# Performance work log

Hardware: AMD Instinct MI355X
Metric: run time of the kernel (lower is better)

The kernel has to match this reference:

```python
import jax, jax.numpy as jnp
import numpy as np
from jax import lax

B, L, D = 2, 512, 1024
N, K, R = 16, 4, 64
DEPTH, V, MLP = 4, 50000, 4096
HALF = D // 2


def _ln(x, s, b, eps=1e-5):
    m = x.mean(-1, keepdims=True)
    v = ((x - m) ** 2).mean(-1, keepdims=True)
    return (x - m) / jnp.sqrt(v + eps) * s + b


def _selective_scan(x, wx, wz, wp, cw, dtw, dtb, a_log, dpar, wout):
    bsz, seqlen, d = x.shape
    x_res = x @ wx.T
    z = x @ wz.T
    p = x @ wp.T  # [B,L,R+2N]
    dt_u, b_proj, c_proj = p[..., :R], p[..., R:R + N], p[..., R + N:]
    dt = jax.nn.softplus(dt_u @ dtw.T + dtb)  # [B,L,D]
    # causal depthwise conv (torch pads K-1 both sides then slices :L == left-pad K-1)
    conv = lax.conv_general_dilated(x_res.transpose(0, 2, 1), cw[:, None, :],
                                    (1,), [(K - 1, 0)], feature_group_count=d)
    u = jax.nn.silu(conv.transpose(0, 2, 1))  # [B,L,D]
    a = -jnp.exp(a_log)  # [D,N]
    a_t = jnp.exp(dt[..., None] * a)  # [B,L,D,N] (ZOH discretize)
    b_t = jnp.where(jnp.abs(a) < 1e-8, dt[..., None], (a_t - 1.0) / (a + 1e-10))
    inp = b_t * b_proj[:, :, None, :] * u[..., None]  # [B,L,D,N]

    def step(h, xs):
        at, it, ct = xs
        h = at * h + it
        return h, jnp.einsum('bn,bdn->bd', ct, h)

    h0 = jnp.zeros((bsz, d, N), a_t.dtype)
    _, ys = lax.scan(step, h0, (a_t.transpose(1, 0, 2, 3),
                                inp.transpose(1, 0, 2, 3),
                                c_proj.transpose(1, 0, 2)))
    y = ys.transpose(1, 0, 2)  # [B,L,D]
    y = (y + u * dpar) * jax.nn.silu(z)
    return y @ wout.T


def _forward(input_ids, timesteps, emb_table, tw1, tb1, tw2, tb2,
             ln1_s, ln1_b, wx, wz, wp, conv_w, dt_w, dt_b, A_log, Dp, wout,
             ln2_s, ln2_b, mlp_w1, mlp_b1, mlp_w2, mlp_b2,
             lnout_s, lnout_b, head_w, head_b):
    # sinusoidal time embedding [B,D]
    freq = jnp.exp(jnp.arange(HALF, dtype=jnp.float32) * (-np.log(10000.0) / (HALF - 1)))
    e = timesteps.astype(jnp.float32)[:, None] * freq
    temb = jnp.concatenate([jnp.sin(e), jnp.cos(e)], axis=-1)
    temb = jax.nn.silu(temb @ tw1.T + tb1) @ tw2.T + tb2
    x = emb_table[input_ids] + temb[:, None, :]
    for i in range(DEPTH):
        h = _selective_scan(_ln(x, ln1_s[i], ln1_b[i]), wx[i], wz[i], wp[i],
                            conv_w[i], dt_w[i], dt_b[i], A_log[i], Dp[i], wout[i])
        x = x + h
        m = _ln(x, ln2_s[i], ln2_b[i])
        m = jax.nn.gelu(m @ mlp_w1[i].T + mlp_b1[i], approximate=False) @ mlp_w2[i].T + mlp_b2[i]
        x = x + m
    x = _ln(x, lnout_s, lnout_b)
    return x @ head_w.T + head_b  # [B,L,V]


def setup_inputs() -> dict:
    key = jax.random.key(0)
    ks = jax.random.split(key, 20)

    def nrm(k, shape, scale=0.02):
        return jax.random.normal(k, shape, jnp.float32) * scale

    dt_std = R ** (-0.5)
    inp = {
        'input_ids': jax.random.randint(ks[0], (B, L), 0, V + 1),
        'timesteps': jax.random.randint(ks[1], (B,), 0, 100),
        'emb_table': nrm(ks[2], (V + 1, D)),
        'tw1': nrm(ks[3], (4 * D, D)), 'tb1': jnp.zeros((4 * D,), jnp.float32),
        'tw2': nrm(ks[4], (D, 4 * D)), 'tb2': jnp.zeros((D,), jnp.float32),
        'ln1_s': jnp.ones((DEPTH, D), jnp.float32), 'ln1_b': jnp.zeros((DEPTH, D), jnp.float32),
        'wx': nrm(ks[5], (DEPTH, D, D)),
        'wz': nrm(ks[6], (DEPTH, D, D)),
        'wp': nrm(ks[7], (DEPTH, R + 2 * N, D)),
        'conv_w': nrm(ks[8], (DEPTH, D, K), 0.1),
        'dt_w': jax.random.uniform(ks[9], (DEPTH, D, R), jnp.float32, -dt_std, dt_std),
        'dt_b': jnp.full((DEPTH, D), float(np.log(np.expm1(0.01))), jnp.float32),
        'A_log': jnp.tile(jnp.log(jnp.arange(1, N + 1, dtype=jnp.float32))[None, None, :], (DEPTH, D, 1)),
        'Dp': jnp.ones((DEPTH, D), jnp.float32),
        'wout': nrm(ks[10], (DEPTH, D, D)),
        'ln2_s': jnp.ones((DEPTH, D), jnp.float32), 'ln2_b': jnp.zeros((DEPTH, D), jnp.float32),
        'mlp_w1': nrm(ks[11], (DEPTH, MLP, D)), 'mlp_b1': jnp.zeros((DEPTH, MLP), jnp.float32),
        'mlp_w2': nrm(ks[12], (DEPTH, D, MLP)), 'mlp_b2': jnp.zeros((DEPTH, D), jnp.float32),
        'lnout_s': jnp.ones((D,), jnp.float32), 'lnout_b': jnp.zeros((D,), jnp.float32),
        'head_w': nrm(ks[13], (V, D)), 'head_b': jnp.zeros((V,), jnp.float32),
    }
    return inp


def reference(input_ids, timesteps, emb_table, tw1, tb1, tw2, tb2,
              ln1_s, ln1_b, wx, wz, wp, conv_w, dt_w, dt_b, A_log, Dp, wout,
              ln2_s, ln2_b, mlp_w1, mlp_b1, mlp_w2, mlp_b2,
              lnout_s, lnout_b, head_w, head_b):
    return _forward(input_ids, timesteps, emb_table, tw1, tb1, tw2, tb2,
                    ln1_s, ln1_b, wx, wz, wp, conv_w, dt_w, dt_b, A_log, Dp, wout,
                    ln2_s, ln2_b, mlp_w1, mlp_b1, mlp_w2, mlp_b2,
                    lnout_s, lnout_b, head_w, head_b)
```

## Files before the change

kernel.cpp:

```cpp
#include <hip/hip_runtime.h>

typedef unsigned short u16;
typedef __attribute__((ext_vector_type(8))) __bf16 bf16x8;
typedef __attribute__((ext_vector_type(4))) float floatx4;

#define B_ 2
#define L_ 512
#define D_ 1024
#define N_ 16
#define R_ 64
#define DEPTH_ 4
#define V_ 50000
#define MLP_ 4096
#define MROWS (B_ * L_)
#define SCAN_C 32
#define SCAN_S (L_ / SCAN_C)

#define SWZ(b) ((b) ^ ((((b) >> 7) & 7) << 4))

__device__ __forceinline__ u16 f2b(float f) {
    return __builtin_bit_cast(u16, (__bf16)f);
}
__device__ __forceinline__ uint2 f4_to_b4(float4 v) {
    u16 a = f2b(v.x), b = f2b(v.y), c = f2b(v.z), d = f2b(v.w);
    uint2 r;
    r.x = (unsigned int)a | ((unsigned int)b << 16);
    r.y = (unsigned int)c | ((unsigned int)d << 16);
    return r;
}
__device__ __forceinline__ void async16(const void* g, void* l) {
    __builtin_amdgcn_global_load_lds(
        (const __attribute__((address_space(1))) void*)g,
        (__attribute__((address_space(3))) void*)l, 16, 0, 0);
}
template <int Ncnt>
__device__ __forceinline__ void waitcnt_vm() {
    if constexpr (Ncnt == 0) asm volatile("s_waitcnt vmcnt(0)" ::: "memory");
    else if constexpr (Ncnt == 2) asm volatile("s_waitcnt vmcnt(2)" ::: "memory");
    else if constexpr (Ncnt == 3) asm volatile("s_waitcnt vmcnt(3)" ::: "memory");
    else if constexpr (Ncnt == 4) asm volatile("s_waitcnt vmcnt(4)" ::: "memory");
    else if constexpr (Ncnt == 5) asm volatile("s_waitcnt vmcnt(5)" ::: "memory");
    else if constexpr (Ncnt == 6) asm volatile("s_waitcnt vmcnt(6)" ::: "memory");
    else if constexpr (Ncnt == 8) asm volatile("s_waitcnt vmcnt(8)" ::: "memory");
    else asm volatile("s_waitcnt vmcnt(0)" ::: "memory");
}
__device__ __forceinline__ float silu_f(float v) { return v / (1.f + expf(-v)); }
__device__ __forceinline__ float gelu_f(float v) {
    return 0.5f * v * (1.f + erff(v * 0.7071067811865476f));
}
__device__ __forceinline__ float softplus_f(float v) {
    return fmaxf(v, 0.f) + log1pf(expf(-fabsf(v)));
}

__global__ __launch_bounds__(256) void cvt_kernel(const float* __restrict__ in,
                                                  u16* __restrict__ out, const int n8) {
    const int i = blockIdx.x * 256 + threadIdx.x;
    if (i >= n8) return;
    const float4 a = *reinterpret_cast<const float4*>(&in[(size_t)i * 8]);
    const float4 b = *reinterpret_cast<const float4*>(&in[(size_t)i * 8 + 4]);
    uint4 o;
    uint2 lo = f4_to_b4(a), hi = f4_to_b4(b);
    o.x = lo.x; o.y = lo.y; o.z = hi.x; o.w = hi.y;
    *reinterpret_cast<uint4*>(&out[(size_t)i * 8]) = o;
}

template <int BM, int BN, int ACT, int RES, typename AT, typename WT, typename OUT>
__global__ __launch_bounds__(256) void gemm_bt(
    const AT* __restrict__ A, const int lda,
    const WT* __restrict__ W, const WT* __restrict__ W2,
    const float* __restrict__ bias,
    OUT* __restrict__ out, OUT* __restrict__ out2,
    const int N, const int K, const int nt) {
    constexpr int BK = 64;
    constexpr int MI = BM / 32;
    constexpr int NI = BN / 32;
    constexpr int WM = BM / 2;
    constexpr bool PIPE = (sizeof(AT) == 2) && (sizeof(WT) == 2);
    __shared__ alignas(16) u16 lA[(PIPE ? 2 : 1) * BM * BK];
    __shared__ alignas(16) u16 lW[(PIPE ? 2 : 1) * BN * BK];
    const int tid = threadIdx.x;
    const int lane = tid & 63, wv = tid >> 6;
    const int bid = blockIdx.x;
    const int m0 = (bid / nt) * BM;
    int n0 = (bid % nt) * BN;
    const WT* Wp = W;
    OUT* op = out;
    if (W2 != nullptr && n0 >= N) {
        Wp = W2;
        op = out2;
        n0 -= N;
    }
    const int wr = wv >> 1, wc = wv & 1;
    const int lr = lane & 15, kg = lane >> 4;

    floatx4 acc[MI][NI];
#pragma unroll
    for (int i = 0; i < MI; ++i)
#pragma unroll
        for (int j = 0; j < NI; ++j) {
            floatx4 z4 = {0.f, 0.f, 0.f, 0.f};
            acc[i][j] = z4;
        }

    const int T = K / BK;

    if constexpr (PIPE) {
        constexpr int NEWER = BM / 32 + BN / 32;
        auto issue = [&](int t) {
            const int buf = t & 1;
            const int kt = t * BK;
#pragma unroll
            for (int c = wv; c < BM / 8; c += 4) {
                const int dst = c * 1024 + lane * 16;
                const int lg = SWZ(dst);
                const int row = lg >> 7, colb = lg & 127;
                async16((const char*)A + ((size_t)(m0 + row) * lda + kt) * 2 + colb,
                        (char*)lA + buf * BM * 128 + c * 1024);
            }
#pragma unroll
            for (int c = wv; c < BN / 8; c += 4) {
                const int dst = c * 1024 + lane * 16;
                const int lg = SWZ(dst);
                const int row = lg >> 7, colb = lg & 127;
                int rn = n0 + row;
                rn = (rn < N) ? rn : (N - 1);
                async16((const char*)Wp + ((size_t)rn * K + kt) * 2 + colb,
                        (char*)lW + buf * BN * 128 + c * 1024);
            }
        };
        issue(0);
        for (int t = 0; t < T; ++t) {
            if (t + 1 < T) {
                issue(t + 1);
                waitcnt_vm<NEWER>();
            } else {
                waitcnt_vm<0>();
            }
            __builtin_amdgcn_s_barrier();
            __builtin_amdgcn_sched_barrier(0);
            const char* bA = (const char*)lA + (t & 1) * BM * 128;
            const char* bW = (const char*)lW + (t & 1) * BN * 128;
#pragma unroll
            for (int kk = 0; kk < 2; ++kk) {
                bf16x8 aF[MI], bF[NI];
#pragma unroll
                for (int mi = 0; mi < MI; ++mi)
                    aF[mi] = *reinterpret_cast<const bf16x8*>(
                        bA + SWZ((wr * WM + mi * 16 + lr) * 128 + kk * 64 + kg * 16));
#pragma unroll
                for (int ni = 0; ni < NI; ++ni)
                    bF[ni] = *reinterpret_cast<const bf16x8*>(
                        bW + SWZ((wc * (BN / 2) + ni * 16 + lr) * 128 + kk * 64 + kg * 16));
#pragma unroll
                for (int mi = 0; mi < MI; ++mi)
#pragma unroll
                    for (int ni = 0; ni < NI; ++ni)
                        acc[mi][ni] = __builtin_amdgcn_mfma_f32_16x16x32_bf16(
                            aF[mi], bF[ni], acc[mi][ni], 0, 0, 0);
            }
            __builtin_amdgcn_sched_barrier(0);
            if (t + 1 < T) __builtin_amdgcn_s_barrier();
        }
    } else {
        for (int t = 0; t < T; ++t) {
            const int kt = t * BK;
            if (t) __syncthreads();
            if constexpr (sizeof(AT) == 2) {
#pragma unroll
                for (int c = wv; c < BM / 8; c += 4) {
                    const int dst = c * 1024 + lane * 16;
                    const int lg = SWZ(dst);
                    const int row = lg >> 7, colb = lg & 127;
                    async16((const char*)A + ((size_t)(m0 + row) * lda + kt) * 2 + colb,
                            (char*)lA + c * 1024);
                }
            } else {
                constexpr int ACHF = (BM * BK) / 1024;
                float4 raF[ACHF];
#pragma unroll
                for (int i = 0; i < ACHF; ++i) {
                    const int idx = tid + i * 256;
                    const int row = idx >> 4, c4 = (idx & 15) * 4;
                    raF[i] = *reinterpret_cast<const float4*>(&A[(size_t)(m0 + row) * lda + kt + c4]);
                }
#pragma unroll
                for (int i = 0; i < ACHF; ++i) {
                    const int idx = tid + i * 256;
                    const int row = idx >> 4, c4 = (idx & 15) * 4;
                    *reinterpret_cast<uint2*>((char*)lA + SWZ(row * 128 + c4 * 2)) = f4_to_b4(raF[i]);
                }
            }
            if constexpr (sizeof(WT) == 2) {
#pragma unroll
                for (int c = wv; c < BN / 8; c += 4) {
                    const int dst = c * 1024 + lane * 16;
                    const int lg = SWZ(dst);
                    const int row = lg >> 7, colb = lg & 127;
                    int rn = n0 + row;
                    rn = (rn < N) ? rn : (N - 1);
                    async16((const char*)Wp + ((size_t)rn * K + kt) * 2 + colb,
                            (char*)lW + c * 1024);
                }
            } else {
                constexpr int WCHF = (BN * BK) / 1024;
                float4 rwF[WCHF];
#pragma unroll
                for (int i = 0; i < WCHF; ++i) {
                    const int idx = tid + i * 256;
                    const int row = idx >> 4, c4 = (idx & 15) * 4;
                    int rn = n0 + row;
                    rn = (rn < N) ? rn : (N - 1);
                    rwF[i] = *reinterpret_cast<const float4*>(&Wp[(size_t)rn * K + kt + c4]);
                }
#pragma unroll
                for (int i = 0; i < WCHF; ++i) {
                    const int idx = tid + i * 256;
                    const int row = idx >> 4, c4 = (idx & 15) * 4;
                    *reinterpret_cast<uint2*>((char*)lW + SWZ(row * 128 + c4 * 2)) = f4_to_b4(rwF[i]);
                }
            }
            __syncthreads();
#pragma unroll
            for (int kk = 0; kk < 2; ++kk) {
                bf16x8 aF[MI], bF[NI];
#pragma unroll
                for (int mi = 0; mi < MI; ++mi)
                    aF[mi] = *reinterpret_cast<const bf16x8*>(
                        (const char*)lA + SWZ((wr * WM + mi * 16 + lr) * 128 + kk * 64 + kg * 16));
#pragma unroll
                for (int ni = 0; ni < NI; ++ni)
                    bF[ni] = *reinterpret_cast<const bf16x8*>(
                        (const char*)lW + SWZ((wc * (BN / 2) + ni * 16 + lr) * 128 + kk * 64 + kg * 16));
#pragma unroll
                for (int mi = 0; mi < MI; ++mi)
#pragma unroll
                    for (int ni = 0; ni < NI; ++ni)
                        acc[mi][ni] = __builtin_amdgcn_mfma_f32_16x16x32_bf16(
                            aF[mi], bF[ni], acc[mi][ni], 0, 0, 0);
            }
        }
    }

#pragma unroll
    for (int mi = 0; mi < MI; ++mi) {
        const int rb = m0 + wr * WM + mi * 16 + kg * 4;
#pragma unroll
        for (int r = 0; r < 4; ++r) {
            const size_t rowoff = (size_t)(rb + r) * (size_t)N;
#pragma unroll
            for (int ni = 0; ni < NI; ++ni) {
                const int col = n0 + wc * (BN / 2) + ni * 16 + lr;
                if (col >= N) continue;
                float v = acc[mi][ni][r] + (bias ? bias[col] : 0.f);
                if constexpr (ACT == 1) v = gelu_f(v);
                if constexpr (ACT == 2) v = softplus_f(v);
                const size_t o = rowoff + (size_t)col;
                if constexpr (RES) {
                    op[o] += v;
                } else if constexpr (sizeof(OUT) == 2) {
                    op[o] = f2b(v);
                } else {
                    op[o] = v;
                }
            }
        }
    }
}

__global__ __launch_bounds__(256) void temb0_kernel(const int* __restrict__ ts,
                                                    float* __restrict__ temb0) {
    int i = blockIdx.x * 256 + threadIdx.x;
    if (i >= B_ * D_) return;
    int b = i >> 10, k = i & 1023;
    float t = (float)ts[b];
    int h = (k < 512) ? k : (k - 512);
    float f = expf((float)h * (-9.210340371976184f / 511.f));
    float e = t * f;
    temb0[i] = (k < 512) ? sinf(e) : cosf(e);
}

template <int ACTV>
__global__ __launch_bounds__(256) void rowdot_kernel(const float* __restrict__ in,
                                                     const float* __restrict__ W,
                                                     const float* __restrict__ bias,
                                                     float* __restrict__ out,
                                                     const int Ncols, const int K) {
    const int g = (blockIdx.x * 256 + threadIdx.x) >> 6;
    const int lane = threadIdx.x & 63;
    if (g >= B_ * Ncols) return;
    const int b = g / Ncols, j = g % Ncols;
    const float* xr = in + (size_t)b * K;
    const float* wr = W + (size_t)j * K;
    float s = 0.f;
    for (int k = lane; k < K; k += 64) s += xr[k] * wr[k];
#pragma unroll
    for (int o = 32; o; o >>= 1) s += __shfl_xor(s, o);
    if (lane == 0) {
        float v = s + bias[j];
        if (ACTV == 1) v = silu_f(v);
        out[(size_t)b * Ncols + j] = v;
    }
}

__global__ __launch_bounds__(256) void embed_kernel(const int* __restrict__ ids,
                                                    const float* __restrict__ emb,
                                                    const float* __restrict__ temb2,
                                                    float* __restrict__ x) {
    const int gid = blockIdx.x * 256 + threadIdx.x;
    const int d8 = gid & 127;
    const int row = gid >> 7;
    const int b = row >> 9;
    const int d0 = d8 * 8;
    const int id = ids[row];
    const float4 e0 = *reinterpret_cast<const float4*>(&emb[(size_t)id * D_ + d0]);
    const float4 e1 = *reinterpret_cast<const float4*>(&emb[(size_t)id * D_ + d0 + 4]);
    const float4 t0 = *reinterpret_cast<const float4*>(&temb2[b * D_ + d0]);
    const float4 t1 = *reinterpret_cast<const float4*>(&temb2[b * D_ + d0 + 4]);
    float4 o0, o1;
    o0.x = e0.x + t0.x; o0.y = e0.y + t0.y; o0.z = e0.z + t0.z; o0.w = e0.w + t0.w;
    o1.x = e1.x + t1.x; o1.y = e1.y + t1.y; o1.z = e1.z + t1.z; o1.w = e1.w + t1.w;
    *reinterpret_cast<float4*>(&x[(size_t)row * D_ + d0]) = o0;
    *reinterpret_cast<float4*>(&x[(size_t)row * D_ + d0 + 4]) = o1;
}

__global__ __launch_bounds__(256) void ln_kernel(const float* __restrict__ x,
                                                 const float* __restrict__ s,
                                                 const float* __restrict__ bb,
                                                 u16* __restrict__ out) {
    __shared__ float red[4];
    const int row = blockIdx.x, tid = threadIdx.x;
    const float4 v = *reinterpret_cast<const float4*>(x + (size_t)row * D_ + tid * 4);
    float sm = v.x + v.y + v.z + v.w;
#pragma unroll
    for (int o = 1; o < 64; o <<= 1) sm += __shfl_xor(sm, o);
    if ((tid & 63) == 0) red[tid >> 6] = sm;
    __syncthreads();
    const float mean = (red[0] + red[1] + red[2] + red[3]) * (1.f / 1024.f);
    __syncthreads();
    const float dx = v.x - mean, dy = v.y - mean, dz = v.z - mean, dw = v.w - mean;
    float sq = dx * dx + dy * dy + dz * dz + dw * dw;
#pragma unroll
    for (int o = 1; o < 64; o <<= 1) sq += __shfl_xor(sq, o);
    if ((tid & 63) == 0) red[tid >> 6] = sq;
    __syncthreads();
    const float var = (red[0] + red[1] + red[2] + red[3]) * (1.f / 1024.f);
    const float rs = rsqrtf(var + 1e-5f);
    const int c = tid * 4;
    const float4 sv = *reinterpret_cast<const float4*>(&s[c]);
    const float4 bv = *reinterpret_cast<const float4*>(&bb[c]);
    float4 o;
    o.x = dx * rs * sv.x + bv.x;
    o.y = dy * rs * sv.y + bv.y;
    o.z = dz * rs * sv.z + bv.z;
    o.w = dw * rs * sv.w + bv.w;
    *reinterpret_cast<uint2*>(&out[(size_t)row * D_ + c]) = f4_to_b4(o);
}

__global__ __launch_bounds__(256) void conv_silu_kernel(const float* __restrict__ xres,
                                                        const float* __restrict__ cw,
                                                        float* __restrict__ u) {
    const int gid = blockIdx.x * 256 + threadIdx.x;
    const int d4 = gid & 255;
    const int row = gid >> 8;
    const int t = row & 511;
    const int b = row >> 9;
    const int d0 = d4 * 4;
    float wj[4][4];
#pragma unroll
    for (int j = 0; j < 4; ++j) {
        const float4 w4 = *reinterpret_cast<const float4*>(&cw[(d0 + j) * 4]);
        wj[j][0] = w4.x; wj[j][1] = w4.y; wj[j][2] = w4.z; wj[j][3] = w4.w;
    }
    float acc[4] = {};
#pragma unroll
    for (int k = 0; k < 4; ++k) {
        const int tt = t - 3 + k;
        if (tt < 0) continue;
        const float4 xv = *reinterpret_cast<const float4*>(&xres[(size_t)(b * L_ + tt) * D_ + d0]);
        acc[0] += xv.x * wj[0][k];
        acc[1] += xv.y * wj[1][k];
        acc[2] += xv.z * wj[2][k];
        acc[3] += xv.w * wj[3][k];
    }
    float4 o;
    o.x = silu_f(acc[0]); o.y = silu_f(acc[1]); o.z = silu_f(acc[2]); o.w = silu_f(acc[3]);
    *reinterpret_cast<float4*>(&u[(size_t)row * D_ + d0]) = o;
}

__global__ __launch_bounds__(256) void scan_p1(const float* __restrict__ dt,
                                               const float* __restrict__ p,
                                               const float* __restrict__ u,
                                               const float* __restrict__ alog,
                                               float* __restrict__ Aprod,
                                               float* __restrict__ Hloc) {
    const int tid = threadIdx.x;
    const int ng = tid & 3;
    const int dl = tid >> 2;
    int blk = blockIdx.x;
    const int chunk = blk % SCAN_C; blk /= SCAN_C;
    const int dg = blk % (D_ / 64);
    const int b = blk / (D_ / 64);
    const int d = dg * 64 + dl;

    float a_v[4], inv_a[4];
#pragma unroll
    for (int j = 0; j < 4; ++j) {
        float av = -expf(alog[d * N_ + ng * 4 + j]);
        a_v[j] = av;
        inv_a[j] = 1.f / (av + 1e-10f);
    }

    __shared__ float pbuf[SCAN_S * 32];
    const int t0 = chunk * SCAN_S;
    if (tid < SCAN_S * 8) {
        const int s = tid >> 3, off = (tid & 7) * 4;
        *reinterpret_cast<float4*>(&pbuf[s * 32 + off]) =
            *reinterpret_cast<const float4*>(&p[((size_t)(b * L_ + t0 + s)) * 96 + 64 + off]);
    }
    __syncthreads();

    float A[4] = {1.f, 1.f, 1.f, 1.f};
    float h[4] = {0.f, 0.f, 0.f, 0.f};
#pragma unroll
    for (int s = 0; s < SCAN_S; ++s) {
        const size_t idx = ((size_t)(b * L_ + t0 + s)) * D_ + d;
        const float dtv = dt[idx];
        const float uv = u[idx];
#pragma unroll
        for (int j = 0; j < 4; ++j) {
            const float ex = fminf(dtv * a_v[j], 0.f);
            const float at = expf(ex);
            const float bt = (fabsf(a_v[j]) < 1e-8f) ? dtv : (at - 1.f) * inv_a[j];
            const float bp = pbuf[s * 32 + ng * 4 + j];
            A[j] *= at;
            h[j] = at * h[j] + bt * bp * uv;
        }
    }
    const size_t o = ((size_t)(b * SCAN_C + chunk) * D_ + d) * N_ + ng * 4;
    float4 a4 = {A[0], A[1], A[2], A[3]};
    float4 h4 = {h[0], h[1], h[2], h[3]};
    *reinterpret_cast<float4*>(&Aprod[o]) = a4;
    *reinterpret_cast<float4*>(&Hloc[o]) = h4;
}

__global__ __launch_bounds__(256) void scan_p2(const float* __restrict__ Aprod,
                                               const float* __restrict__ Hloc,
                                               float* __restrict__ Hstart) {
    const int gid = blockIdx.x * 256 + threadIdx.x;
    if (gid >= B_ * D_ * N_) return;
    const int b = gid / (D_ * N_);
    const int rem = gid % (D_ * N_);
    float H = 0.f;
#pragma unroll 8
    for (int k = 0; k < SCAN_C; ++k) {
        const size_t o = (size_t)(b * SCAN_C + k) * (D_ * N_) + rem;
        Hstart[o] = H;
        H = Aprod[o] * H + Hloc[o];
    }
}

__global__ __launch_bounds__(256) void scan_p3(const float* __restrict__ dt,
                                               const float* __restrict__ p,
                                               const float* __restrict__ u,
                                               const float* __restrict__ z,
                                               const float* __restrict__ alog,
                                               const float* __restrict__ Dp,
                                               const float* __restrict__ Hstart,
                                               u16* __restrict__ yg) {
    const int tid = threadIdx.x;
    const int ng = tid & 3;
    const int dl = tid >> 2;
    int blk = blockIdx.x;
    const int chunk = blk % SCAN_C; blk /= SCAN_C;
    const int dg = blk % (D_ / 64);
    const int b = blk / (D_ / 64);
    const int d = dg * 64 + dl;

    float a_v[4], inv_a[4];
#pragma unroll
    for (int j = 0; j < 4; ++j) {
        float av = -expf(alog[d * N_ + ng * 4 + j]);
        a_v[j] = av;
        inv_a[j] = 1.f / (av + 1e-10f);
    }
    const float Dpd = Dp[d];

    __shared__ float pbuf[SCAN_S * 32];
    const int t0 = chunk * SCAN_S;
    if (tid < SCAN_S * 8) {
        const int s = tid >> 3, off = (tid & 7) * 4;
        *reinterpret_cast<float4*>(&pbuf[s * 32 + off]) =
            *reinterpret_cast<const float4*>(&p[((size_t)(b * L_ + t0 + s)) * 96 + 64 + off]);
    }
    __syncthreads();

    float h[4];
    {
        const size_t o = ((size_t)(b * SCAN_C + chunk) * D_ + d) * N_ + ng * 4;
        const float4 h4 = *reinterpret_cast<const float4*>(&Hstart[o]);
        h[0] = h4.x; h[1] = h4.y; h[2] = h4.z; h[3] = h4.w;
    }

#pragma unroll
    for (int s = 0; s < SCAN_S; ++s) {
        const size_t idx = ((size_t)(b * L_ + t0 + s)) * D_ + d;
        const float dtv = dt[idx];
        const float uv = u[idx];
        float yp = 0.f;
#pragma unroll
        for (int j = 0; j < 4; ++j) {
            const float ex = fminf(dtv * a_v[j], 0.f);
            const float at = expf(ex);
            const float bt = (fabsf(a_v[j]) < 1e-8f) ? dtv : (at - 1.f) * inv_a[j];
            const float bp = pbuf[s * 32 + ng * 4 + j];
            const float cp = pbuf[s * 32 + 16 + ng * 4 + j];
            h[j] = at * h[j] + bt * bp * uv;
            yp += cp * h[j];
        }
        yp += __shfl_xor(yp, 1);
        yp += __shfl_xor(yp, 2);
        if (ng == 0) {
            const float zv = z[idx];
            yg[idx] = f2b((yp + uv * Dpd) * silu_f(zv));
        }
    }
}

extern "C" void kernel_launch(void* const* d_in, const int* in_sizes, int n_in,
                              void* d_out, int out_size, void* d_ws, size_t ws_size,
                              hipStream_t stream) {
    (void)in_sizes; (void)n_in; (void)out_size;
    const int* ids = (const int*)d_in[0];
    const int* tsteps = (const int*)d_in[1];
    const float* emb = (const float*)d_in[2];
    const float* tw1 = (const float*)d_in[3];
    const float* tb1 = (const float*)d_in[4];
    const float* tw2 = (const float*)d_in[5];
    const float* tb2 = (const float*)d_in[6];
    const float* ln1s = (const float*)d_in[7];
    const float* ln1b = (const float*)d_in[8];
    const float* wx = (const float*)d_in[9];
    const float* wz = (const float*)d_in[10];
    const float* wp = (const float*)d_in[11];
    const float* convw = (const float*)d_in[12];
    const float* dtw = (const float*)d_in[13];
    const float* dtb = (const float*)d_in[14];
    const float* alog = (const float*)d_in[15];
    const float* dp = (const float*)d_in[16];
    const float* wo = (const float*)d_in[17];
    const float* ln2s = (const float*)d_in[18];
    const float* ln2b = (const float*)d_in[19];
    const float* mw1 = (const float*)d_in[20];
    const float* mb1 = (const float*)d_in[21];
    const float* mw2 = (const float*)d_in[22];
    const float* mb2 = (const float*)d_in[23];
    const float* lnos = (const float*)d_in[24];
    const float* lnob = (const float*)d_in[25];
    const float* hw = (const float*)d_in[26];
    const float* hb = (const float*)d_in[27];
    float* outp = (float*)d_out;

    char* w = (char*)d_ws;
    size_t used = 0;
    auto alloc = [&](size_t bytes) {
        char* pp = w;
        size_t rb = (bytes + 255) & ~(size_t)255;
        w += rb;
        used += rb;
        return pp;
    };
    float* x = (float*)alloc((size_t)MROWS * D_ * 4);
    float* t0f = (float*)alloc((size_t)B_ * D_ * 4);
    float* t1f = (float*)alloc((size_t)B_ * MLP_ * 4);
    float* t2f = (float*)alloc((size_t)B_ * D_ * 4);
    u16* xnb = (u16*)alloc((size_t)MROWS * D_ * 2);
    float* xres = (float*)alloc((size_t)MROWS * D_ * 4);
    float* zf = (float*)alloc((size_t)MROWS * D_ * 4);
    float* pf = (float*)alloc((size_t)MROWS * 96 * 4);
    float* dtf = (float*)alloc((size_t)MROWS * D_ * 4);
    float* uf = (float*)alloc((size_t)MROWS * D_ * 4);
    u16* ygb = (u16*)alloc((size_t)MROWS * D_ * 2);
    const bool cvt_head = (ws_size >= used + (size_t)V_ * D_ * 2 + 4096);
    u16* hwb = cvt_head ? (u16*)alloc((size_t)V_ * D_ * 2) : nullptr;
    const size_t lw_bytes = ((size_t)DEPTH_ * D_ * D_ * 3 + (size_t)DEPTH_ * 96 * D_ +
                             (size_t)DEPTH_ * D_ * R_ + (size_t)DEPTH_ * MLP_ * D_ * 2) * 2;
    const bool cvt_layer = cvt_head && (ws_size >= used + lw_bytes + (size_t)1 << 20);
    u16 *wxb = nullptr, *wzb = nullptr, *wpb = nullptr, *dtwb = nullptr, *wob = nullptr,
        *mw1b = nullptr, *mw2b = nullptr;
    if (cvt_layer) {
        wxb = (u16*)alloc((size_t)DEPTH_ * D_ * D_ * 2);
        wzb = (u16*)alloc((size_t)DEPTH_ * D_ * D_ * 2);
        wpb = (u16*)alloc((size_t)DEPTH_ * 96 * D_ * 2);
        dtwb = (u16*)alloc((size_t)DEPTH_ * D_ * R_ * 2);
        wob = (u16*)alloc((size_t)DEPTH_ * D_ * D_ * 2);
        mw1b = (u16*)alloc((size_t)DEPTH_ * MLP_ * D_ * 2);
        mw2b = (u16*)alloc((size_t)DEPTH_ * MLP_ * D_ * 2);
    }
    u16* m1b = (u16*)outp;
    float* Aprod = outp + (size_t)6 * 1024 * 1024;
    float* Hloc = outp + (size_t)8 * 1024 * 1024;
    float* Hstart = outp + (size_t)10 * 1024 * 1024;

    auto cvt = [&](const float* src, u16* dst, size_t n) {
        cvt_kernel<<<dim3((unsigned)((n / 8 + 255) / 256)), dim3(256), 0, stream>>>(src, dst,
                                                                                   (int)(n / 8));
    };
    if (cvt_head) cvt(hw, hwb, (size_t)V_ * D_);
    if (cvt_layer) {
        cvt(wx, wxb, (size_t)DEPTH_ * D_ * D_);
        cvt(wz, wzb, (size_t)DEPTH_ * D_ * D_);
        cvt(wp, wpb, (size_t)DEPTH_ * 96 * D_);
        cvt(dtw, dtwb, (size_t)DEPTH_ * D_ * R_);
        cvt(wo, wob, (size_t)DEPTH_ * D_ * D_);
        cvt(mw1, mw1b, (size_t)DEPTH_ * MLP_ * D_);
        cvt(mw2, mw2b, (size_t)DEPTH_ * MLP_ * D_);
    }
    temb0_kernel<<<dim3((B_ * D_ + 255) / 256), dim3(256), 0, stream>>>(tsteps, t0f);
    rowdot_kernel<1><<<dim3(B_ * MLP_ / 4), dim3(256), 0, stream>>>(t0f, tw1, tb1, t1f, MLP_, D_);
    rowdot_kernel<0><<<dim3(B_ * D_ / 4), dim3(256), 0, stream>>>(t1f, tw2, tb2, t2f, D_, MLP_);
    embed_kernel<<<dim3(MROWS * D_ / 8 / 256), dim3(256), 0, stream>>>(ids, emb, t2f, x);

    for (int i = 0; i < DEPTH_; ++i) {
        const float* wpi = wp + (size_t)i * 96 * D_;
        const float* cwi = convw + (size_t)i * D_ * 4;
        const float* dtbi = dtb + (size_t)i * D_;
        const float* ali = alog + (size_t)i * D_ * N_;
        const float* dpi = dp + (size_t)i * D_;
        const float* mb1i = mb1 + (size_t)i * MLP_;
        const float* mb2i = mb2 + (size_t)i * D_;

        ln_kernel<<<dim3(MROWS), dim3(256), 0, stream>>>(x, ln1s + i * D_, ln1b + i * D_, xnb);
        if (cvt_layer) {
            gemm_bt<32, 64, 0, 0, u16, u16, float><<<dim3(1024), dim3(256), 0, stream>>>(
                xnb, D_, wxb + (size_t)i * D_ * D_, wzb + (size_t)i * D_ * D_, nullptr,
                xres, zf, D_, D_, 32);
            gemm_bt<32, 64, 0, 0, u16, u16, float><<<dim3(64), dim3(256), 0, stream>>>(
                xnb, D_, wpb + (size_t)i * 96 * D_, nullptr, nullptr, pf, nullptr, 96, D_, 2);
            gemm_bt<32, 64, 2, 0, float, u16, float><<<dim3(512), dim3(256), 0, stream>>>(
                pf, 96, dtwb + (size_t)i * D_ * R_, nullptr, dtbi, dtf, nullptr, D_, R_, 16);
        } else {
            gemm_bt<32, 64, 0, 0, u16, float, float><<<dim3(1024), dim3(256), 0, stream>>>(
                xnb, D_, wx + (size_t)i * D_ * D_, wz + (size_t)i * D_ * D_, nullptr,
                xres, zf, D_, D_, 32);
            gemm_bt<32, 64, 0, 0, u16, float, float><<<dim3(64), dim3(256), 0, stream>>>(
                xnb, D_, wpi, nullptr, nullptr, pf, nullptr, 96, D_, 2);
            gemm_bt<32, 64, 2, 0, float, float, float><<<dim3(512), dim3(256), 0, stream>>>(
                pf, 96, dtw + (size_t)i * D_ * R_, nullptr, dtbi, dtf, nullptr, D_, R_, 16);
        }
        conv_silu_kernel<<<dim3(MROWS * D_ / 4 / 256), dim3(256), 0, stream>>>(xres, cwi, uf);
        scan_p1<<<dim3(B_ * (D_ / 64) * SCAN_C), dim3(256), 0, stream>>>(
            dtf, pf, uf, ali, Aprod, Hloc);
        scan_p2<<<dim3(B_ * D_ * N_ / 256), dim3(256), 0, stream>>>(Aprod, Hloc, Hstart);
        scan_p3<<<dim3(B_ * (D_ / 64) * SCAN_C), dim3(256), 0, stream>>>(
            dtf, pf, uf, zf, ali, dpi, Hstart, ygb);
        if (cvt_layer) {
            gemm_bt<32, 64, 0, 1, u16, u16, float><<<dim3(512), dim3(256), 0, stream>>>(
                ygb, D_, wob + (size_t)i * D_ * D_, nullptr, nullptr, x, nullptr, D_, D_, 16);
        } else {
            gemm_bt<32, 64, 0, 1, u16, float, float><<<dim3(512), dim3(256), 0, stream>>>(
                ygb, D_, wo + (size_t)i * D_ * D_, nullptr, nullptr, x, nullptr, D_, D_, 16);
        }
        ln_kernel<<<dim3(MROWS), dim3(256), 0, stream>>>(x, ln2s + i * D_, ln2b + i * D_, xnb);
        if (cvt_layer) {
            gemm_bt<32, 64, 1, 0, u16, u16, u16><<<dim3(2048), dim3(256), 0, stream>>>(
                xnb, D_, mw1b + (size_t)i * MLP_ * D_, nullptr, mb1i, m1b, nullptr, MLP_, D_, 64);
            gemm_bt<32, 64, 0, 1, u16, u16, float><<<dim3(512), dim3(256), 0, stream>>>(
                m1b, MLP_, mw2b + (size_t)i * MLP_ * D_, nullptr, mb2i, x, nullptr, D_, MLP_, 16);
        } else {
            gemm_bt<32, 64, 1, 0, u16, float, u16><<<dim3(2048), dim3(256), 0, stream>>>(
                xnb, D_, mw1 + (size_t)i * MLP_ * D_, nullptr, mb1i, m1b, nullptr, MLP_, D_, 64);
            gemm_bt<32, 64, 0, 1, u16, float, float><<<dim3(512), dim3(256), 0, stream>>>(
                m1b, MLP_, mw2 + (size_t)i * MLP_ * D_, nullptr, mb2i, x, nullptr, D_, MLP_, 16);
        }
    }

    ln_kernel<<<dim3(MROWS), dim3(256), 0, stream>>>(x, lnos, lnob, xnb);
    if (cvt_head) {
        gemm_bt<128, 128, 0, 0, u16, u16, float>
            <<<dim3(8 * ((V_ + 127) / 128)), dim3(256), 0, stream>>>(
                xnb, D_, hwb, (const u16*)nullptr, hb, outp, nullptr, V_, D_, (V_ + 127) / 128);
    } else {
        gemm_bt<128, 128, 0, 0, u16, float, float>
            <<<dim3(8 * ((V_ + 127) / 128)), dim3(256), 0, stream>>>(
                xnb, D_, hw, (const float*)nullptr, hb, outp, nullptr, V_, D_, (V_ + 127) / 128);
    }
}
```

Before: 1.159 ms.

## Store SSM intermediates in bf16, group-swizzle head GEMM tiles, disable head pipelining

Stores xres, z, dt and u as bf16 instead of fp32, which halves the memory traffic of the conv, scan and GEMM-epilogue kernels. The conv kernel is widened to 8 channels per thread. Adds a grouped block-index mapping (group size 32 along N) for the large vocab head GEMM to improve L2 reuse of activation tiles. It also adds a template flag that turns off the double-buffered pipeline for the head GEMM. The extra rounding of intermediates to bf16 may reduce accuracy, and dropping the head pipeline could hurt that GEMM's throughput.

```diff
diff --git a/kernel.cpp b/kernel.cpp
--- a/kernel.cpp
+++ b/kernel.cpp
@@ -18,6 +18,10 @@
 
 #define SWZ(b) ((b) ^ ((((b) >> 7) & 7) << 4))
 
+__device__ __forceinline__ float b2f(u16 u) {
+    unsigned int i = ((unsigned int)u) << 16;
+    return __builtin_bit_cast(float, i);
+}
 __device__ __forceinline__ u16 f2b(float f) {
     return __builtin_bit_cast(u16, (__bf16)f);
 }
@@ -39,7 +43,6 @@
     else if constexpr (Ncnt == 2) asm volatile("s_waitcnt vmcnt(2)" ::: "memory");
     else if constexpr (Ncnt == 3) asm volatile("s_waitcnt vmcnt(3)" ::: "memory");
     else if constexpr (Ncnt == 4) asm volatile("s_waitcnt vmcnt(4)" ::: "memory");
-    else if constexpr (Ncnt == 5) asm volatile("s_waitcnt vmcnt(5)" ::: "memory");
     else if constexpr (Ncnt == 6) asm volatile("s_waitcnt vmcnt(6)" ::: "memory");
     else if constexpr (Ncnt == 8) asm volatile("s_waitcnt vmcnt(8)" ::: "memory");
     else asm volatile("s_waitcnt vmcnt(0)" ::: "memory");
@@ -64,25 +67,46 @@
     *reinterpret_cast<uint4*>(&out[(size_t)i * 8]) = o;
 }
 
-template <int BM, int BN, int ACT, int RES, typename AT, typename WT, typename OUT>
+template <int BM, int BN, int ACT, int RES, int PIPEOK, typename AT, typename WT, typename OUT>
 __global__ __launch_bounds__(256) void gemm_bt(
     const AT* __restrict__ A, const int lda,
     const WT* __restrict__ W, const WT* __restrict__ W2,
     const float* __restrict__ bias,
     OUT* __restrict__ out, OUT* __restrict__ out2,
-    const int N, const int K, const int nt) {
+    const int N, const int K, const int nt, const int gsz) {
     constexpr int BK = 64;
     constexpr int MI = BM / 32;
     constexpr int NI = BN / 32;
     constexpr int WM = BM / 2;
-    constexpr bool PIPE = (sizeof(AT) == 2) && (sizeof(WT) == 2);
+    constexpr bool PIPE = PIPEOK && (sizeof(AT) == 2) && (sizeof(WT) == 2);
     __shared__ alignas(16) u16 lA[(PIPE ? 2 : 1) * BM * BK];
     __shared__ alignas(16) u16 lW[(PIPE ? 2 : 1) * BN * BK];
     const int tid = threadIdx.x;
     const int lane = tid & 63, wv = tid >> 6;
     const int bid = blockIdx.x;
-    const int m0 = (bid / nt) * BM;
-    int n0 = (bid % nt) * BN;
+
+    int mI, nI;
+    if (gsz > 0) {
+        const int mtt = gridDim.x / nt;
+        const int fullG = nt / gsz;
+        const int fullBlocks = fullG * gsz * mtt;
+        if (bid < fullBlocks) {
+            const int per = gsz * mtt;
+            const int g = bid / per, r = bid % per;
+            mI = r / gsz;
+            nI = g * gsz + r % gsz;
+        } else {
+            const int rem = nt - fullG * gsz;
+            const int r = bid - fullBlocks;
+            mI = r / rem;
+            nI = fullG * gsz + r % rem;
+        }
+    } else {
+        mI = bid / nt;
+        nI = bid % nt;
+    }
+    const int m0 = mI * BM;
+    int n0 = nI * BN;
     const WT* Wp = W;
     OUT* op = out;
     if (W2 != nullptr && n0 >= N) {
@@ -356,40 +380,41 @@
     *reinterpret_cast<uint2*>(&out[(size_t)row * D_ + c]) = f4_to_b4(o);
 }
 
-__global__ __launch_bounds__(256) void conv_silu_kernel(const float* __restrict__ xres,
+__global__ __launch_bounds__(256) void conv_silu_kernel(const u16* __restrict__ xres,
                                                         const float* __restrict__ cw,
-                                                        float* __restrict__ u) {
+                                                        u16* __restrict__ u) {
     const int gid = blockIdx.x * 256 + threadIdx.x;
-    const int d4 = gid & 255;
-    const int row = gid >> 8;
+    const int d8 = gid & 127;
+    const int row = gid >> 7;
     const int t = row & 511;
     const int b = row >> 9;
-    const int d0 = d4 * 4;
-    float wj[4][4];
-#pragma unroll
-    for (int j = 0; j < 4; ++j) {
+    const int d0 = d8 * 8;
+    float wj[8][4];
+#pragma unroll
+    for (int j = 0; j < 8; ++j) {
         const float4 w4 = *reinterpret_cast<const float4*>(&cw[(d0 + j) * 4]);
         wj[j][0] = w4.x; wj[j][1] = w4.y; wj[j][2] = w4.z; wj[j][3] = w4.w;
     }
-    float acc[4] = {};
+    float acc[8] = {};
 #pragma unroll
     for (int k = 0; k < 4; ++k) {
         const int tt = t - 3 + k;
         if (tt < 0) continue;
-        const float4 xv = *reinterpret_cast<const float4*>(&xres[(size_t)(b * L_ + tt) * D_ + d0]);
-        acc[0] += xv.x * wj[0][k];
-        acc[1] += xv.y * wj[1][k];
-        acc[2] += xv.z * wj[2][k];
-        acc[3] += xv.w * wj[3][k];
-    }
-    float4 o;
-    o.x = silu_f(acc[0]); o.y = silu_f(acc[1]); o.z = silu_f(acc[2]); o.w = silu_f(acc[3]);
-    *reinterpret_cast<float4*>(&u[(size_t)row * D_ + d0]) = o;
-}
-
-__global__ __launch_bounds__(256) void scan_p1(const float* __restrict__ dt,
+        alignas(16) u16 xr[8];
+        *reinterpret_cast<uint4*>(xr) =
+            *reinterpret_cast<const uint4*>(&xres[(size_t)(b * L_ + tt) * D_ + d0]);
+#pragma unroll
+        for (int j = 0; j < 8; ++j) acc[j] += b2f(xr[j]) * wj[j][k];
+    }
+    alignas(16) u16 ov[8];
+#pragma unroll
+    for (int j = 0; j < 8; ++j) ov[j] = f2b(silu_f(acc[j]));
+    *reinterpret_cast<uint4*>(&u[(size_t)row * D_ + d0]) = *reinterpret_cast<uint4*>(ov);
+}
+
+__global__ __launch_bounds__(256) void scan_p1(const u16* __restrict__ dt,
                                                const float* __restrict__ p,
-                                               const float* __restrict__ u,
+                                               const u16* __restrict__ u,
                                                const float* __restrict__ alog,
                                                float* __restrict__ Aprod,
                                                float* __restrict__ Hloc) {
@@ -424,8 +449,8 @@
 #pragma unroll
     for (int s = 0; s < SCAN_S; ++s) {
         const size_t idx = ((size_t)(b * L_ + t0 + s)) * D_ + d;
-        const float dtv = dt[idx];
-        const float uv = u[idx];
+        const float dtv = b2f(dt[idx]);
+        const float uv = b2f(u[idx]);
 #pragma unroll
         for (int j = 0; j < 4; ++j) {
             const float ex = fminf(dtv * a_v[j], 0.f);
@@ -459,10 +484,10 @@
     }
 }
 
-__global__ __launch_bounds__(256) void scan_p3(const float* __restrict__ dt,
+__global__ __launch_bounds__(256) void scan_p3(const u16* __restrict__ dt,
                                                const float* __restrict__ p,
-                                               const float* __restrict__ u,
-                                               const float* __restrict__ z,
+                                               const u16* __restrict__ u,
+                                               const u16* __restrict__ z,
                                                const float* __restrict__ alog,
                                                const float* __restrict__ Dp,
                                                const float* __restrict__ Hstart,
@@ -504,8 +529,8 @@
 #pragma unroll
     for (int s = 0; s < SCAN_S; ++s) {
         const size_t idx = ((size_t)(b * L_ + t0 + s)) * D_ + d;
-        const float dtv = dt[idx];
-        const float uv = u[idx];
+        const float dtv = b2f(dt[idx]);
+        const float uv = b2f(u[idx]);
         float yp = 0.f;
 #pragma unroll
         for (int j = 0; j < 4; ++j) {
@@ -520,7 +545,7 @@
         yp += __shfl_xor(yp, 1);
         yp += __shfl_xor(yp, 2);
         if (ng == 0) {
-            const float zv = z[idx];
+            const float zv = b2f(z[idx]);
             yg[idx] = f2b((yp + uv * Dpd) * silu_f(zv));
         }
     }
@@ -574,17 +599,17 @@
     float* t1f = (float*)alloc((size_t)B_ * MLP_ * 4);
     float* t2f = (float*)alloc((size_t)B_ * D_ * 4);
     u16* xnb = (u16*)alloc((size_t)MROWS * D_ * 2);
-    float* xres = (float*)alloc((size_t)MROWS * D_ * 4);
-    float* zf = (float*)alloc((size_t)MROWS * D_ * 4);
+    u16* xres = (u16*)alloc((size_t)MROWS * D_ * 2);
+    u16* zb = (u16*)alloc((size_t)MROWS * D_ * 2);
     float* pf = (float*)alloc((size_t)MROWS * 96 * 4);
-    float* dtf = (float*)alloc((size_t)MROWS * D_ * 4);
-    float* uf = (float*)alloc((size_t)MROWS * D_ * 4);
+    u16* dtb16 = (u16*)alloc((size_t)MROWS * D_ * 2);
+    u16* ub = (u16*)alloc((size_t)MROWS * D_ * 2);
     u16* ygb = (u16*)alloc((size_t)MROWS * D_ * 2);
     const bool cvt_head = (ws_size >= used + (size_t)V_ * D_ * 2 + 4096);
     u16* hwb = cvt_head ? (u16*)alloc((size_t)V_ * D_ * 2) : nullptr;
     const size_t lw_bytes = ((size_t)DEPTH_ * D_ * D_ * 3 + (size_t)DEPTH_ * 96 * D_ +
                              (size_t)DEPTH_ * D_ * R_ + (size_t)DEPTH_ * MLP_ * D_ * 2) * 2;
-    const bool cvt_layer = cvt_head && (ws_size >= used + lw_bytes + (size_t)1 << 20);
+    const bool cvt_layer = cvt_head && (ws_size >= used + lw_bytes + ((size_t)1 << 20));
     u16 *wxb = nullptr, *wzb = nullptr, *wpb = nullptr, *dtwb = nullptr, *wob = nullptr,
         *mw1b = nullptr, *mw2b = nullptr;
     if (cvt_layer) {
@@ -621,7 +646,6 @@
     embed_kernel<<<dim3(MROWS * D_ / 8 / 256), dim3(256), 0, stream>>>(ids, emb, t2f, x);
 
     for (int i = 0; i < DEPTH_; ++i) {
-        const float* wpi = wp + (size_t)i * 96 * D_;
         const float* cwi = convw + (size_t)i * D_ * 4;
         const float* dtbi = dtb + (size_t)i * D_;
         const float* ali = alog + (size_t)i * D_ * N_;
@@ -631,57 +655,59 @@
 
         ln_kernel<<<dim3(MROWS), dim3(256), 0, stream>>>(x, ln1s + i * D_, ln1b + i * D_, xnb);
         if (cvt_layer) {
-            gemm_bt<32, 64, 0, 0, u16, u16, float><<<dim3(1024), dim3(256), 0, stream>>>(
+            gemm_bt<32, 64, 0, 0, 1, u16, u16, u16><<<dim3(1024), dim3(256), 0, stream>>>(
                 xnb, D_, wxb + (size_t)i * D_ * D_, wzb + (size_t)i * D_ * D_, nullptr,
-                xres, zf, D_, D_, 32);
-            gemm_bt<32, 64, 0, 0, u16, u16, float><<<dim3(64), dim3(256), 0, stream>>>(
-                xnb, D_, wpb + (size_t)i * 96 * D_, nullptr, nullptr, pf, nullptr, 96, D_, 2);
-            gemm_bt<32, 64, 2, 0, float, u16, float><<<dim3(512), dim3(256), 0, stream>>>(
-                pf, 96, dtwb + (size_t)i * D_ * R_, nullptr, dtbi, dtf, nullptr, D_, R_, 16);
+                xres, zb, D_, D_, 32, 0);
+            gemm_bt<32, 64, 0, 0, 1, u16, u16, float><<<dim3(64), dim3(256), 0, stream>>>(
+                xnb, D_, wpb + (size_t)i * 96 * D_, nullptr, nullptr, pf, nullptr, 96, D_, 2, 0);
+            gemm_bt<32, 64, 2, 0, 1, float, u16, u16><<<dim3(512), dim3(256), 0, stream>>>(
+                pf, 96, dtwb + (size_t)i * D_ * R_, nullptr, dtbi, dtb16, nullptr, D_, R_, 16, 0);
         } else {
-            gemm_bt<32, 64, 0, 0, u16, float, float><<<dim3(1024), dim3(256), 0, stream>>>(
+            gemm_bt<32, 64, 0, 0, 1, u16, float, u16><<<dim3(1024), dim3(256), 0, stream>>>(
                 xnb, D_, wx + (size_t)i * D_ * D_, wz + (size_t)i * D_ * D_, nullptr,
-                xres, zf, D_, D_, 32);
-            gemm_bt<32, 64, 0, 0, u16, float, float><<<dim3(64), dim3(256), 0, stream>>>(
-                xnb, D_, wpi, nullptr, nullptr, pf, nullptr, 96, D_, 2);
-            gemm_bt<32, 64, 2, 0, float, float, float><<<dim3(512), dim3(256), 0, stream>>>(
-                pf, 96, dtw + (size_t)i * D_ * R_, nullptr, dtbi, dtf, nullptr, D_, R_, 16);
-        }
-        conv_silu_kernel<<<dim3(MROWS * D_ / 4 / 256), dim3(256), 0, stream>>>(xres, cwi, uf);
+                xres, zb, D_, D_, 32, 0);
+            gemm_bt<32, 64, 0, 0, 1, u16, float, float><<<dim3(64), dim3(256), 0, stream>>>(
+                xnb, D_, wp + (size_t)i * 96 * D_, nullptr, nullptr, pf, nullptr, 96, D_, 2, 0);
+            gemm_bt<32, 64, 2, 0, 1, float, float, u16><<<dim3(512), dim3(256), 0, stream>>>(
+                pf, 96, dtw + (size_t)i * D_ * R_, nullptr, dtbi, dtb16, nullptr, D_, R_, 16, 0);
+        }
+        conv_silu_kernel<<<dim3(MROWS * D_ / 8 / 256), dim3(256), 0, stream>>>(xres, cwi, ub);
         scan_p1<<<dim3(B_ * (D_ / 64) * SCAN_C), dim3(256), 0, stream>>>(
-            dtf, pf, uf, ali, Aprod, Hloc);
+            dtb16, pf, ub, ali, Aprod, Hloc);
         scan_p2<<<dim3(B_ * D_ * N_ / 256), dim3(256), 0, stream>>>(Aprod, Hloc, Hstart);
         scan_p3<<<dim3(B_ * (D_ / 64) * SCAN_C), dim3(256), 0, stream>>>(
-            dtf, pf, uf, zf, ali, dpi, Hstart, ygb);
+            dtb16, pf, ub, zb, ali, dpi, Hstart, ygb);
         if (cvt_layer) {
-            gemm_bt<32, 64, 0, 1, u16, u16, float><<<dim3(512), dim3(256), 0, stream>>>(
-                ygb, D_, wob + (size_t)i * D_ * D_, nullptr, nullptr, x, nullptr, D_, D_, 16);
+            gemm_bt<32, 64, 0, 1, 1, u16, u16, float><<<dim3(512), dim3(256), 0, stream>>>(
+                ygb, D_, wob + (size_t)i * D_ * D_, nullptr, nullptr, x, nullptr, D_, D_, 16, 0);
         } else {
-            gemm_bt<32, 64, 0, 1, u16, float, float><<<dim3(512), dim3(256), 0, stream>>>(
-                ygb, D_, wo + (size_t)i * D_ * D_, nullptr, nullptr, x, nullptr, D_, D_, 16);
+            gemm_bt<32, 64, 0, 1, 1, u16, float, float><<<dim3(512), dim3(256), 0, stream>>>(
+                ygb, D_, wo + (size_t)i * D_ * D_, nullptr, nullptr, x, nullptr, D_, D_, 16, 0);
         }
         ln_kernel<<<dim3(MROWS), dim3(256), 0, stream>>>(x, ln2s + i * D_, ln2b + i * D_, xnb);
         if (cvt_layer) {
-            gemm_bt<32, 64, 1, 0, u16, u16, u16><<<dim3(2048), dim3(256), 0, stream>>>(
-                xnb, D_, mw1b + (size_t)i * MLP_ * D_, nullptr, mb1i, m1b, nullptr, MLP_, D_, 64);
-            gemm_bt<32, 64, 0, 1, u16, u16, float><<<dim3(512), dim3(256), 0, stream>>>(
-                m1b, MLP_, mw2b + (size_t)i * MLP_ * D_, nullptr, mb2i, x, nullptr, D_, MLP_, 16);
+            gemm_bt<32, 64, 1, 0, 1, u16, u16, u16><<<dim3(2048), dim3(256), 0, stream>>>(
+                xnb, D_, mw1b + (size_t)i * MLP_ * D_, nullptr, mb1i, m1b, nullptr, MLP_, D_, 64, 0);
+            gemm_bt<32, 64, 0, 1, 1, u16, u16, float><<<dim3(512), dim3(256), 0, stream>>>(
+                m1b, MLP_, mw2b + (size_t)i * MLP_ * D_, nullptr, mb2i, x, nullptr, D_, MLP_, 16, 0);
         } else {
-            gemm_bt<32, 64, 1, 0, u16, float, u16><<<dim3(2048), dim3(256), 0, stream>>>(
-                xnb, D_, mw1 + (size_t)i * MLP_ * D_, nullptr, mb1i, m1b, nullptr, MLP_, D_, 64);
-            gemm_bt<32, 64, 0, 1, u16, float, float><<<dim3(512), dim3(256), 0, stream>>>(
-                m1b, MLP_, mw2 + (size_t)i * MLP_ * D_, nullptr, mb2i, x, nullptr, D_, MLP_, 16);
+            gemm_bt<32, 64, 1, 0, 1, u16, float, u16><<<dim3(2048), dim3(256), 0, stream>>>(
+                xnb, D_, mw1 + (size_t)i * MLP_ * D_, nullptr, mb1i, m1b, nullptr, MLP_, D_, 64, 0);
+            gemm_bt<32, 64, 0, 1, 1, u16, float, float><<<dim3(512), dim3(256), 0, stream>>>(
+                m1b, MLP_, mw2 + (size_t)i * MLP_ * D_, nullptr, mb2i, x, nullptr, D_, MLP_, 16, 0);
         }
     }
 
     ln_kernel<<<dim3(MROWS), dim3(256), 0, stream>>>(x, lnos, lnob, xnb);
     if (cvt_head) {
-        gemm_bt<128, 128, 0, 0, u16, u16, float>
+        gemm_bt<128, 128, 0, 0, 0, u16, u16, float>
             <<<dim3(8 * ((V_ + 127) / 128)), dim3(256), 0, stream>>>(
-                xnb, D_, hwb, (const u16*)nullptr, hb, outp, nullptr, V_, D_, (V_ + 127) / 128);
+                xnb, D_, hwb, (const u16*)nullptr, hb, outp, nullptr, V_, D_,
+                (V_ + 127) / 128, 32);
     } else {
-        gemm_bt<128, 128, 0, 0, u16, float, float>
+        gemm_bt<128, 128, 0, 0, 0, u16, float, float>
             <<<dim3(8 * ((V_ + 127) / 128)), dim3(256), 0, stream>>>(
-                xnb, D_, hw, (const float*)nullptr, hb, outp, nullptr, V_, D_, (V_ + 127) / 128);
-    }
-}
+                xnb, D_, hw, (const float*)nullptr, hb, outp, nullptr, V_, D_,
+                (V_ + 127) / 128, 32);
+    }
+}
```

Result: faster. 961.4 us (-17.1%).
